# Performance work log

Measured on AMD Instinct MI355X. Metric: run time of the kernel, lower is better.

The kernel has to match this reference:

```python
import jax, jax.numpy as jnp
import numpy as np

B = 262144
NUM_FEA = 32
EMB_DIM = 8
OUT_DIM = 16

def setup_inputs() -> dict:
    key = jax.random.key(0)
    ks = jax.random.split(key, 6)
    x = jax.random.normal(ks[0], (B, NUM_FEA), dtype=jnp.float32)
    # per-feature Dense(1 -> emb_dim): weight row + bias per feature
    emb_W = jax.random.normal(ks[1], (NUM_FEA, EMB_DIM), dtype=jnp.float32) * 0.5
    emb_b = jax.random.normal(ks[2], (NUM_FEA, EMB_DIM), dtype=jnp.float32) * 0.1
    M = jax.random.normal(ks[3], (EMB_DIM, EMB_DIM), dtype=jnp.float32) * (1.0 / np.sqrt(EMB_DIM))
    dense_W = jax.random.normal(ks[4], (NUM_FEA, OUT_DIM), dtype=jnp.float32) * (1.0 / np.sqrt(NUM_FEA))
    dense_b = jax.random.normal(ks[5], (OUT_DIM,), dtype=jnp.float32) * 0.1
    return {"x": x, "emb_W": emb_W, "emb_b": emb_b, "M": M,
            "dense_W": dense_W, "dense_b": dense_b}

def reference(x, emb_W, emb_b, M, dense_W, dense_b):
    mid = x.shape[1] // 2  # 16
    # fused batched per-feature Dense(1 -> emb_dim): [B, F, E]
    emb = x[:, :, None] * emb_W[None, :, :] + emb_b[None, :, :]
    left = emb[:, :mid, :]    # [B, mid, E]
    right = emb[:, mid:, :]   # [B, mid, E]
    # bilinear co-attention: G = tanh(left @ M @ right^T), [B, mid, mid]
    G = jnp.tanh(jnp.einsum('ble,ef,brf->blr', left, M, right))
    lr = jax.nn.softmax(G.sum(axis=1), axis=-1)  # [B, mid]
    rl = jax.nn.softmax(G.sum(axis=2), axis=-1)  # [B, mid]
    a = jnp.concatenate([lr, rl], axis=-1)       # [B, F]
    out = x * a
    # mix == 'concat': Dense(16, relu)
    return jax.nn.relu(out @ dense_W + dense_b)
```

## Files before the change

kernel.cpp:

```cpp
#include <hip/hip_runtime.h>
#include <hip/hip_bf16.h>


typedef __attribute__((ext_vector_type(2))) float v2f;

#if __has_builtin(__builtin_amdgcn_exp2f)
#define EXP2F(v) __builtin_amdgcn_exp2f(v)
#else
#define EXP2F(v) exp2f(v)
#endif

#if __has_builtin(__builtin_amdgcn_rcpf)
#define RCPF(v) __builtin_amdgcn_rcpf(v)
#else
#define RCPF(v) (1.0f / (v))
#endif

#define LOG2E 1.4426950408889634f

__device__ __forceinline__ v2f fma2(v2f a, v2f b, v2f c) {
    return __builtin_elementwise_fma(a, b, c);
}

__global__ __launch_bounds__(256) void coattn_setup(
    const float* __restrict__ emb_W,
    const float* __restrict__ emb_b,
    const float* __restrict__ M,
    float* __restrict__ C)
{
    const int t = threadIdx.x;
    const int l = t >> 4;
    const int r = t & 15;

    float MW[8], Mb[8];
    #pragma unroll
    for (int e = 0; e < 8; ++e) {
        float s1 = 0.0f, s2 = 0.0f;
        #pragma unroll
        for (int f = 0; f < 8; ++f) {
            float m = M[e * 8 + f];
            s1 = fmaf(m, emb_W[(16 + r) * 8 + f], s1);
            s2 = fmaf(m, emb_b[(16 + r) * 8 + f], s2);
        }
        MW[e] = s1; Mb[e] = s2;
    }
    float c1 = 0.0f, c2 = 0.0f, c3 = 0.0f, c4 = 0.0f;
    #pragma unroll
    for (int e = 0; e < 8; ++e) {
        float w = emb_W[l * 8 + e];
        float b = emb_b[l * 8 + e];
        c1 = fmaf(w, MW[e], c1);
        c2 = fmaf(w, Mb[e], c2);
        c3 = fmaf(b, MW[e], c3);
        c4 = fmaf(b, Mb[e], c4);
    }
    const float s = 2.0f * LOG2E;
    C[0 * 256 + l * 16 + r] = c1 * s;
    C[1 * 256 + l * 16 + r] = c2 * s;
    C[2 * 256 + l * 16 + r] = c3 * s;
    C[3 * 256 + l * 16 + r] = c4 * s;
}

template<int P>
__device__ __forceinline__ void dense_tail(
    const v2f (&xl2)[4], const v2f (&xr2)[8], const v2f (&elr)[8],
    float invlr, float invrl, const float (&er)[8],
    const v2f* __restrict__ dW2, const v2f* __restrict__ db2v,
    v2f* __restrict__ slot,
    v2f& r0, v2f& r1, v2f& r2, v2f& r3)
{
    v2f xa[8];
    #pragma unroll
    for (int i = 0; i < 4; ++i)
        xa[i] = xl2[i] * (elr[4 * P + i] * invlr);
    #pragma unroll
    for (int i = 0; i < 4; ++i) {
        v2f a; a.x = er[2 * i] * invrl; a.y = er[2 * i + 1] * invrl;
        xa[4 + i] = xr2[4 * P + i] * a;
    }

    v2f o2[8];
    #pragma unroll
    for (int m = 0; m < 8; ++m) o2[m] = (v2f){0.0f, 0.0f};
    #pragma unroll
    for (int m = 0; m < 4; ++m) o2[4 * P + m] = db2v[4 * P + m];

    #pragma unroll
    for (int i2 = 0; i2 < 8; ++i2) {
        const float xj = xa[i2 >> 1][i2 & 1];
        const v2f xj2 = (v2f){xj, xj};
        const v2f* row = dW2 + (8 * P + i2) * 8;
        #pragma unroll
        for (int m = 0; m < 8; ++m) o2[m] = fma2(xj2, row[m], o2[m]);
    }
    #pragma unroll
    for (int i2 = 0; i2 < 8; ++i2) {
        const float xj = xa[4 + (i2 >> 1)][i2 & 1];
        const v2f xj2 = (v2f){xj, xj};
        const v2f* row = dW2 + (16 + 8 * P + i2) * 8;
        #pragma unroll
        for (int m = 0; m < 8; ++m) o2[m] = fma2(xj2, row[m], o2[m]);
    }

    #pragma unroll
    for (int m = 0; m < 4; ++m) slot[m] = o2[4 * (1 - P) + m];
    r0 = o2[4 * P + 0]; r1 = o2[4 * P + 1];
    r2 = o2[4 * P + 2]; r3 = o2[4 * P + 3];
}

__global__ __launch_bounds__(128, 8) void coattn_kernel(
    const float* __restrict__ x,
    const float* __restrict__ C,
    const float* __restrict__ dW,
    const float* __restrict__ db,
    float* __restrict__ out)
{
    #pragma clang fp contract(off)

    __shared__ float ldsS[128 * 16];
    __shared__ float ldsP[128];

    const int tid  = threadIdx.x;
    const int lane = tid & 63;
    const int p    = __builtin_amdgcn_readfirstlane(tid >> 6);
    const long e   = (long)blockIdx.x * 64 + lane;

    v2f xl2[4], xr2[8];
    {
        const float4* xp = reinterpret_cast<const float4*>(x + e * 32);
        float4 a0 = xp[2 * p], a1 = xp[2 * p + 1];
        xl2[0] = (v2f){a0.x, a0.y}; xl2[1] = (v2f){a0.z, a0.w};
        xl2[2] = (v2f){a1.x, a1.y}; xl2[3] = (v2f){a1.z, a1.w};
        #pragma unroll
        for (int k = 0; k < 4; ++k) {
            float4 v = xp[4 + k];
            xr2[2*k] = (v2f){v.x, v.y}; xr2[2*k+1] = (v2f){v.z, v.w};
        }
    }

    const v2f* C1 = reinterpret_cast<const v2f*>(C) + p * 64;
    const v2f* C2 = reinterpret_cast<const v2f*>(C) + 128 + p * 64;
    const v2f* C3 = reinterpret_cast<const v2f*>(C) + 256 + p * 64;
    const v2f* C4 = reinterpret_cast<const v2f*>(C) + 384 + p * 64;

    v2f Scol[8];
    #pragma unroll
    for (int k = 0; k < 8; ++k) Scol[k] = (v2f){0.0f, 0.0f};
    float Srow[8];

    #pragma unroll
    for (int l = 0; l < 8; ++l) {
        const float xl_ = xl2[l >> 1][l & 1];
        const v2f xlv = (v2f){xl_, xl_};
        v2f rs = (v2f){0.0f, 0.0f};
        #pragma unroll
        for (int k = 0; k < 8; ++k) {
            v2f u = xlv * C1[l * 8 + k]; u = u + C3[l * 8 + k];
            v2f w = xlv * C2[l * 8 + k]; w = w + C4[l * 8 + k];
            v2f g = fma2(xr2[k], u, w);
            v2f E; E.x = EXP2F(g.x); E.y = EXP2F(g.y);
            v2f D = E + 1.0f;
            v2f rc; rc.x = RCPF(D.x); rc.y = RCPF(D.y);
            Scol[k] = Scol[k] + rc;
            rs = rs + rc;
        }
        Srow[l] = rs.x + rs.y;
    }

    const float NSCL = -2.0f * LOG2E;
    float er[8], pd = 0.0f;
    #pragma unroll
    for (int l = 0; l < 8; ++l) { er[l] = EXP2F(Srow[l] * NSCL); pd += er[l]; }

    {
        v2f* myS = reinterpret_cast<v2f*>(ldsS + tid * 16);
        #pragma unroll
        for (int k = 0; k < 8; ++k) myS[k] = Scol[k];
        ldsP[tid] = pd;
    }
    __syncthreads();
    float denr;
    {
        const int q = tid ^ 64;
        const v2f* pS = reinterpret_cast<const v2f*>(ldsS + q * 16);
        #pragma unroll
        for (int k = 0; k < 8; ++k) Scol[k] = Scol[k] + pS[k];
        denr = pd + ldsP[q];
    }

    v2f elr[8];
    float s = 0.0f;
    #pragma unroll
    for (int k = 0; k < 8; ++k) {
        v2f arg = Scol[k] * NSCL;
        v2f ee; ee.x = EXP2F(arg.x); ee.y = EXP2F(arg.y);
        elr[k] = ee;
        s += ee.x + ee.y;
    }
    const float invlr = RCPF(s);
    const float invrl = RCPF(denr);

    __syncthreads();

    const v2f* dW2  = reinterpret_cast<const v2f*>(dW);
    const v2f* db2v = reinterpret_cast<const v2f*>(db);
    v2f* slot = reinterpret_cast<v2f*>(ldsS + tid * 16);
    v2f r0, r1, r2, r3;
    if (p == 0)
        dense_tail<0>(xl2, xr2, elr, invlr, invrl, er, dW2, db2v, slot, r0, r1, r2, r3);
    else
        dense_tail<1>(xl2, xr2, elr, invlr, invrl, er, dW2, db2v, slot, r0, r1, r2, r3);

    __syncthreads();

    {
        const v2f* ps = reinterpret_cast<const v2f*>(ldsS + (tid ^ 64) * 16);
        v2f z = (v2f){0.0f, 0.0f};
        v2f f0 = __builtin_elementwise_max(r0 + ps[0], z);
        v2f f1 = __builtin_elementwise_max(r1 + ps[1], z);
        v2f f2 = __builtin_elementwise_max(r2 + ps[2], z);
        v2f f3 = __builtin_elementwise_max(r3 + ps[3], z);
        float4* op = reinterpret_cast<float4*>(out + e * 16 + p * 8);
        float4 v0; v0.x = f0.x; v0.y = f0.y; v0.z = f1.x; v0.w = f1.y;
        float4 v1; v1.x = f2.x; v1.y = f2.y; v1.z = f3.x; v1.w = f3.y;
        op[0] = v0;
        op[1] = v1;
    }
}

extern "C" void kernel_launch(void* const* d_in, const int* in_sizes, int n_in,
                              void* d_out, int out_size, void* d_ws, size_t ws_size,
                              hipStream_t stream) {
    const float* x     = (const float*)d_in[0];
    const float* emb_W = (const float*)d_in[1];
    const float* emb_b = (const float*)d_in[2];
    const float* M     = (const float*)d_in[3];
    const float* dW    = (const float*)d_in[4];
    const float* db    = (const float*)d_in[5];
    float* out = (float*)d_out;
    float* C   = (float*)d_ws;

    hipLaunchKernelGGL(coattn_setup, dim3(1), dim3(256), 0, stream,
                       emb_W, emb_b, M, C);

    const int B = in_sizes[0] / 32;
    dim3 block(128);
    dim3 grid(B / 64);
    hipLaunchKernelGGL(coattn_kernel, grid, block, 0, stream,
                       x, C, dW, db, out);
}
```

Before: 106.8 us.

## Split each row's co-attention across four waves with padded LDS reductions

Each batch row is now handled by four wavefronts instead of two. Each wave computes 4 of the 16 left rows of the attention grid, and column sums, row-softmax denominators and the dense partial outputs are combined through a padded (stride-18) LDS buffer. The pairwise reciprocals are replaced by one reciprocal of the product plus two multiplies, with the exponent argument clamped to avoid overflow. This cuts per-thread transcendental and ALU work and raises parallelism. In exchange it adds more LDS traffic and synchronisation, and drops the occupancy hint in the launch bounds.

```diff
diff --git a/kernel.cpp b/kernel.cpp
--- a/kernel.cpp
+++ b/kernel.cpp
@@ -61,54 +61,7 @@
     C[3 * 256 + l * 16 + r] = c4 * s;
 }
 
-template<int P>
-__device__ __forceinline__ void dense_tail(
-    const v2f (&xl2)[4], const v2f (&xr2)[8], const v2f (&elr)[8],
-    float invlr, float invrl, const float (&er)[8],
-    const v2f* __restrict__ dW2, const v2f* __restrict__ db2v,
-    v2f* __restrict__ slot,
-    v2f& r0, v2f& r1, v2f& r2, v2f& r3)
-{
-    v2f xa[8];
-    #pragma unroll
-    for (int i = 0; i < 4; ++i)
-        xa[i] = xl2[i] * (elr[4 * P + i] * invlr);
-    #pragma unroll
-    for (int i = 0; i < 4; ++i) {
-        v2f a; a.x = er[2 * i] * invrl; a.y = er[2 * i + 1] * invrl;
-        xa[4 + i] = xr2[4 * P + i] * a;
-    }
-
-    v2f o2[8];
-    #pragma unroll
-    for (int m = 0; m < 8; ++m) o2[m] = (v2f){0.0f, 0.0f};
-    #pragma unroll
-    for (int m = 0; m < 4; ++m) o2[4 * P + m] = db2v[4 * P + m];
-
-    #pragma unroll
-    for (int i2 = 0; i2 < 8; ++i2) {
-        const float xj = xa[i2 >> 1][i2 & 1];
-        const v2f xj2 = (v2f){xj, xj};
-        const v2f* row = dW2 + (8 * P + i2) * 8;
-        #pragma unroll
-        for (int m = 0; m < 8; ++m) o2[m] = fma2(xj2, row[m], o2[m]);
-    }
-    #pragma unroll
-    for (int i2 = 0; i2 < 8; ++i2) {
-        const float xj = xa[4 + (i2 >> 1)][i2 & 1];
-        const v2f xj2 = (v2f){xj, xj};
-        const v2f* row = dW2 + (16 + 8 * P + i2) * 8;
-        #pragma unroll
-        for (int m = 0; m < 8; ++m) o2[m] = fma2(xj2, row[m], o2[m]);
-    }
-
-    #pragma unroll
-    for (int m = 0; m < 4; ++m) slot[m] = o2[4 * (1 - P) + m];
-    r0 = o2[4 * P + 0]; r1 = o2[4 * P + 1];
-    r2 = o2[4 * P + 2]; r3 = o2[4 * P + 3];
-}
-
-__global__ __launch_bounds__(128, 8) void coattn_kernel(
+__global__ __launch_bounds__(256) void coattn_kernel(
     const float* __restrict__ x,
     const float* __restrict__ C,
     const float* __restrict__ dW,
@@ -117,115 +70,153 @@
 {
     #pragma clang fp contract(off)
 
-    __shared__ float ldsS[128 * 16];
-    __shared__ float ldsP[128];
+    __shared__ float ldsS[256 * 18];
+    __shared__ float ldsP[256];
 
     const int tid  = threadIdx.x;
     const int lane = tid & 63;
-    const int p    = __builtin_amdgcn_readfirstlane(tid >> 6);
+    const int w    = __builtin_amdgcn_readfirstlane(tid >> 6);
     const long e   = (long)blockIdx.x * 64 + lane;
-
-    v2f xl2[4], xr2[8];
+    const float* xe = x + e * 32;
+
+    v2f xl2[2], xr2[8], xrl2[2];
     {
-        const float4* xp = reinterpret_cast<const float4*>(x + e * 32);
-        float4 a0 = xp[2 * p], a1 = xp[2 * p + 1];
-        xl2[0] = (v2f){a0.x, a0.y}; xl2[1] = (v2f){a0.z, a0.w};
-        xl2[2] = (v2f){a1.x, a1.y}; xl2[3] = (v2f){a1.z, a1.w};
+        float4 t0 = *reinterpret_cast<const float4*>(xe + 4 * w);
+        xl2[0] = (v2f){t0.x, t0.y}; xl2[1] = (v2f){t0.z, t0.w};
         #pragma unroll
         for (int k = 0; k < 4; ++k) {
-            float4 v = xp[4 + k];
+            float4 v = *reinterpret_cast<const float4*>(xe + 16 + 4 * k);
             xr2[2*k] = (v2f){v.x, v.y}; xr2[2*k+1] = (v2f){v.z, v.w};
         }
-    }
-
-    const v2f* C1 = reinterpret_cast<const v2f*>(C) + p * 64;
-    const v2f* C2 = reinterpret_cast<const v2f*>(C) + 128 + p * 64;
-    const v2f* C3 = reinterpret_cast<const v2f*>(C) + 256 + p * 64;
-    const v2f* C4 = reinterpret_cast<const v2f*>(C) + 384 + p * 64;
+        float4 t1 = *reinterpret_cast<const float4*>(xe + 16 + 4 * w);
+        xrl2[0] = (v2f){t1.x, t1.y}; xrl2[1] = (v2f){t1.z, t1.w};
+    }
+
+    const v2f* Cv = reinterpret_cast<const v2f*>(C);
 
     v2f Scol[8];
     #pragma unroll
     for (int k = 0; k < 8; ++k) Scol[k] = (v2f){0.0f, 0.0f};
-    float Srow[8];
-
-    #pragma unroll
-    for (int l = 0; l < 8; ++l) {
-        const float xl_ = xl2[l >> 1][l & 1];
-        const v2f xlv = (v2f){xl_, xl_};
+    float er[4];
+    float pd = 0.0f;
+    const float NSCL = -2.0f * LOG2E;
+
+    #pragma unroll
+    for (int i = 0; i < 4; ++i) {
+        const int l = 4 * w + i;
+        const float xls = xl2[i >> 1][i & 1];
+        const v2f xlv = (v2f){xls, xls};
         v2f rs = (v2f){0.0f, 0.0f};
         #pragma unroll
         for (int k = 0; k < 8; ++k) {
-            v2f u = xlv * C1[l * 8 + k]; u = u + C3[l * 8 + k];
-            v2f w = xlv * C2[l * 8 + k]; w = w + C4[l * 8 + k];
-            v2f g = fma2(xr2[k], u, w);
+            v2f c1 = Cv[0 * 128 + l * 8 + k];
+            v2f c2 = Cv[1 * 128 + l * 8 + k];
+            v2f c3 = Cv[2 * 128 + l * 8 + k];
+            v2f c4 = Cv[3 * 128 + l * 8 + k];
+            v2f u = xlv * c1; u = u + c3;
+            v2f q = xlv * c2; q = q + c4;
+            v2f g = fma2(xr2[k], u, q);
+            g = __builtin_elementwise_min(g, (v2f){88.0f, 88.0f});
             v2f E; E.x = EXP2F(g.x); E.y = EXP2F(g.y);
             v2f D = E + 1.0f;
-            v2f rc; rc.x = RCPF(D.x); rc.y = RCPF(D.y);
+            float P = D.x * D.y;
+            float t = RCPF(P);
+            v2f rc; rc.x = D.y * t; rc.y = D.x * t;
             Scol[k] = Scol[k] + rc;
             rs = rs + rc;
         }
-        Srow[l] = rs.x + rs.y;
-    }
-
-    const float NSCL = -2.0f * LOG2E;
-    float er[8], pd = 0.0f;
-    #pragma unroll
-    for (int l = 0; l < 8; ++l) { er[l] = EXP2F(Srow[l] * NSCL); pd += er[l]; }
-
-    {
-        v2f* myS = reinterpret_cast<v2f*>(ldsS + tid * 16);
-        #pragma unroll
-        for (int k = 0; k < 8; ++k) myS[k] = Scol[k];
-        ldsP[tid] = pd;
-    }
+        float srow = rs.x + rs.y;
+        er[i] = EXP2F(srow * NSCL);
+        pd += er[i];
+    }
+
+    float* slot = ldsS + tid * 18;
+    #pragma unroll
+    for (int k = 0; k < 8; ++k) *reinterpret_cast<v2f*>(slot + 2 * k) = Scol[k];
+    ldsP[tid] = pd;
     __syncthreads();
-    float denr;
-    {
-        const int q = tid ^ 64;
-        const v2f* pS = reinterpret_cast<const v2f*>(ldsS + q * 16);
-        #pragma unroll
-        for (int k = 0; k < 8; ++k) Scol[k] = Scol[k] + pS[k];
-        denr = pd + ldsP[q];
-    }
-
-    v2f elr[8];
+
+    float denr = pd;
+    #pragma unroll
+    for (int p = 1; p < 4; ++p) {
+        const int q = ((w + p) & 3) * 64 + lane;
+        const float* ps = ldsS + q * 18;
+        #pragma unroll
+        for (int k = 0; k < 8; ++k)
+            Scol[k] = Scol[k] + *reinterpret_cast<const v2f*>(ps + 2 * k);
+        denr += ldsP[q];
+    }
     float s = 0.0f;
     #pragma unroll
     for (int k = 0; k < 8; ++k) {
         v2f arg = Scol[k] * NSCL;
-        v2f ee; ee.x = EXP2F(arg.x); ee.y = EXP2F(arg.y);
-        elr[k] = ee;
-        s += ee.x + ee.y;
+        s += EXP2F(arg.x) + EXP2F(arg.y);
     }
     const float invlr = RCPF(s);
     const float invrl = RCPF(denr);
 
+    v2f q0 = (v2f){0.0f, 0.0f}, q1 = (v2f){0.0f, 0.0f};
+    #pragma unroll
+    for (int wp = 0; wp < 4; ++wp) {
+        const float* ps = ldsS + (wp * 64 + lane) * 18 + 4 * w;
+        q0 = q0 + *reinterpret_cast<const v2f*>(ps);
+        q1 = q1 + *reinterpret_cast<const v2f*>(ps + 2);
+    }
+    v2f elrq0; elrq0.x = EXP2F(q0.x * NSCL); elrq0.y = EXP2F(q0.y * NSCL);
+    v2f elrq1; elrq1.x = EXP2F(q1.x * NSCL); elrq1.y = EXP2F(q1.y * NSCL);
+
     __syncthreads();
+
+    v2f xa0 = xl2[0] * (elrq0 * invlr);
+    v2f xa1 = xl2[1] * (elrq1 * invlr);
+    v2f ar0; ar0.x = er[0] * invrl; ar0.y = er[1] * invrl;
+    v2f ar1; ar1.x = er[2] * invrl; ar1.y = er[3] * invrl;
+    v2f xb0 = xrl2[0] * ar0;
+    v2f xb1 = xrl2[1] * ar1;
 
     const v2f* dW2  = reinterpret_cast<const v2f*>(dW);
     const v2f* db2v = reinterpret_cast<const v2f*>(db);
-    v2f* slot = reinterpret_cast<v2f*>(ldsS + tid * 16);
-    v2f r0, r1, r2, r3;
-    if (p == 0)
-        dense_tail<0>(xl2, xr2, elr, invlr, invrl, er, dW2, db2v, slot, r0, r1, r2, r3);
-    else
-        dense_tail<1>(xl2, xr2, elr, invlr, invrl, er, dW2, db2v, slot, r0, r1, r2, r3);
-
+    v2f o2[8];
+    if (w == 0) {
+        #pragma unroll
+        for (int m = 0; m < 8; ++m) o2[m] = db2v[m];
+    } else {
+        #pragma unroll
+        for (int m = 0; m < 8; ++m) o2[m] = (v2f){0.0f, 0.0f};
+    }
+    #pragma unroll
+    for (int i = 0; i < 4; ++i) {
+        const float xj = (i < 2 ? xa0 : xa1)[i & 1];
+        const v2f xj2 = (v2f){xj, xj};
+        const v2f* row = dW2 + (4 * w + i) * 8;
+        #pragma unroll
+        for (int m = 0; m < 8; ++m) o2[m] = fma2(xj2, row[m], o2[m]);
+    }
+    #pragma unroll
+    for (int i = 0; i < 4; ++i) {
+        const float xj = (i < 2 ? xb0 : xb1)[i & 1];
+        const v2f xj2 = (v2f){xj, xj};
+        const v2f* row = dW2 + (16 + 4 * w + i) * 8;
+        #pragma unroll
+        for (int m = 0; m < 8; ++m) o2[m] = fma2(xj2, row[m], o2[m]);
+    }
+
+    #pragma unroll
+    for (int m = 0; m < 8; ++m) *reinterpret_cast<v2f*>(slot + 2 * m) = o2[m];
     __syncthreads();
 
-    {
-        const v2f* ps = reinterpret_cast<const v2f*>(ldsS + (tid ^ 64) * 16);
-        v2f z = (v2f){0.0f, 0.0f};
-        v2f f0 = __builtin_elementwise_max(r0 + ps[0], z);
-        v2f f1 = __builtin_elementwise_max(r1 + ps[1], z);
-        v2f f2 = __builtin_elementwise_max(r2 + ps[2], z);
-        v2f f3 = __builtin_elementwise_max(r3 + ps[3], z);
-        float4* op = reinterpret_cast<float4*>(out + e * 16 + p * 8);
-        float4 v0; v0.x = f0.x; v0.y = f0.y; v0.z = f1.x; v0.w = f1.y;
-        float4 v1; v1.x = f2.x; v1.y = f2.y; v1.z = f3.x; v1.w = f3.y;
-        op[0] = v0;
-        op[1] = v1;
-    }
+    v2f f0 = (v2f){0.0f, 0.0f}, f1 = (v2f){0.0f, 0.0f};
+    #pragma unroll
+    for (int wp = 0; wp < 4; ++wp) {
+        const float* ps = ldsS + (wp * 64 + lane) * 18 + 4 * w;
+        f0 = f0 + *reinterpret_cast<const v2f*>(ps);
+        f1 = f1 + *reinterpret_cast<const v2f*>(ps + 2);
+    }
+    const v2f z = (v2f){0.0f, 0.0f};
+    f0 = __builtin_elementwise_max(f0, z);
+    f1 = __builtin_elementwise_max(f1, z);
+    float4 v; v.x = f0.x; v.y = f0.y; v.z = f1.x; v.w = f1.y;
+    *reinterpret_cast<float4*>(out + e * 16 + 4 * w) = v;
 }
 
 extern "C" void kernel_launch(void* const* d_in, const int* in_sizes, int n_in,
@@ -244,7 +235,7 @@
                        emb_W, emb_b, M, C);
 
     const int B = in_sizes[0] / 32;
-    dim3 block(128);
+    dim3 block(256);
     dim3 grid(B / 64);
     hipLaunchKernelGGL(coattn_kernel, grid, block, 0, stream,
                        x, C, dW, db, out);
```

Result: no change. 106.7 us (-0.2%).
